# Performance work log

Hardware: AMD Instinct MI355X
Metric: run time of the kernel (lower is better)

The kernel has to match this reference:

```python
import jax, jax.numpy as jnp
import numpy as np
from jax import lax

N, C_IN, L = 32, 8, 4096
C_LAT, K_EMB, E_DIM = 64, 512, 64
KSZ, STRIDE, PAD = 4, 2, 2


def setup_inputs() -> dict:
    key = jax.random.key(0)
    ks = jax.random.split(key, 6)
    s_conv = 1.0 / np.sqrt(C_IN * KSZ)
    s_tconv = 1.0 / np.sqrt(C_LAT * KSZ)
    return {
        "x": jax.random.normal(ks[0], (N, C_IN, L), jnp.float32),
        "conv_w": jax.random.normal(ks[1], (C_LAT, C_IN, KSZ), jnp.float32) * s_conv,
        "conv_b": jax.random.normal(ks[2], (C_LAT,), jnp.float32) * s_conv,
        "codebook": jax.random.normal(ks[3], (K_EMB, E_DIM), jnp.float32),
        "tconv_w": jax.random.normal(ks[4], (C_LAT, C_IN, KSZ), jnp.float32) * s_tconv,
        "tconv_b": jax.random.normal(ks[5], (C_IN,), jnp.float32) * s_tconv,
    }


def _encode(x, conv_w, conv_b):
    z = lax.conv_general_dilated(
        x, conv_w, window_strides=(STRIDE,), padding=[(PAD, PAD)],
        dimension_numbers=("NCH", "OIH", "NCH"))
    return z + conv_b[None, :, None]


def _quantize(z_e, codebook):
    n, c, l = z_e.shape
    z_flat = z_e.transpose(0, 2, 1).reshape(-1, c)          # (n*l, c)
    z_sq = jnp.sum(z_flat * z_flat, axis=1, keepdims=True)  # (n*l, 1)
    cb_sq = jnp.sum(codebook * codebook, axis=1)            # (k,)
    dist = z_sq + cb_sq[None, :] - 2.0 * (z_flat @ codebook.T)
    indices = jnp.argmin(dist, axis=-1)                     # (n*l,)
    z_q = codebook[indices].reshape(n, l, c).transpose(0, 2, 1)
    return z_q, indices.reshape(n, l)


def _decode(z_q, tconv_w, tconv_b):
    # torch ConvTranspose1d == conv with lhs-dilated input, flipped/transposed kernel
    w_t = jnp.flip(tconv_w, -1).transpose(1, 0, 2)          # (out, in, k)
    x_rec = lax.conv_general_dilated(
        z_q, w_t, window_strides=(1,),
        padding=[(KSZ - 1 - PAD, KSZ - 1 - PAD)],
        lhs_dilation=(STRIDE,),
        dimension_numbers=("NCH", "OIH", "NCH"))
    return x_rec + tconv_b[None, :, None]


def reference(x, conv_w, conv_b, codebook, tconv_w, tconv_b):
    z_e = _encode(x, conv_w, conv_b)            # (N, C_LAT, L/2+1)
    z_q, indices = _quantize(z_e, codebook)
    x_recon = _decode(z_q, tconv_w, tconv_b)    # (N, C_IN, L)
    return x_recon, z_e, z_q, indices
```

## Files before the change

### kernel.cpp

```cpp
#include <hip/hip_runtime.h>
#include <stdint.h>

#define N_B   32
#define C_INN 8
#define L_IN  4096
#define C_LAT 64
#define K_EMB 512
#define E_DIM 64
#define L_OUT 2049
#define M_ROWS (N_B * L_OUT)

#define SZ_XREC (N_B * C_INN * L_IN)
#define SZ_ZE   (N_B * C_LAT * L_OUT)
#define OFF_XREC 0
#define OFF_ZE   (SZ_XREC)
#define OFF_ZQ   (OFF_ZE + SZ_ZE)
#define OFF_IDX  (OFF_ZQ + SZ_ZE)

typedef short short8 __attribute__((ext_vector_type(8)));
typedef float f32x4  __attribute__((ext_vector_type(4)));

__device__ __forceinline__ unsigned short rne16(float f) {
    unsigned u = __float_as_uint(f);
    return (unsigned short)((u + 0x7FFFu + ((u >> 16) & 1u)) >> 16);
}
__device__ __forceinline__ float frombits16(unsigned short h) {
    return __uint_as_float(((unsigned)h) << 16);
}
__device__ __forceinline__ unsigned orderbits(float f) {
    unsigned u = __float_as_uint(f);
    return u ^ ((unsigned)((int)u >> 31) | 0x80000000u);
}

__global__ __launch_bounds__(256) void prep_kernel(
    const float* __restrict__ cb, unsigned short* __restrict__ frag,
    float* __restrict__ cbh)
{
    const int ntile = blockIdx.x;
    const int t     = threadIdx.x;
    const int lane  = t & 63;
    const int ks    = (t >> 6) & 1;
    const int h     = t >> 7;
    const int code  = ntile * 16 + (lane & 15);
    const int k0    = ks * 32 + (lane >> 4) * 8;

    const float* src = cb + (size_t)code * E_DIM + k0;
    unsigned short out[8];
#pragma unroll
    for (int j = 0; j < 8; ++j) {
        const float v = src[j];
        const unsigned short hb = rne16(v);
        out[j] = h ? rne16(v - frombits16(hb)) : hb;
    }
    short8 v8;
#pragma unroll
    for (int j = 0; j < 8; ++j) v8[j] = (short)out[j];
    short8* dst = (short8*)(frag + (((size_t)(ntile * 2 + ks) * 2 + h) * 512 + lane * 8));
    *dst = v8;

    if (t < 16) {
        const int c2 = ntile * 16 + t;
        const float4* cp = (const float4*)(cb + (size_t)c2 * E_DIM);
        float s = 0.0f;
#pragma unroll
        for (int d = 0; d < E_DIM / 4; ++d) {
            float4 v = cp[d];
            s += v.x * v.x + v.y * v.y + v.z * v.z + v.w * v.w;
        }
        cbh[c2] = 0.5f * s;
    }
}

__global__ __launch_bounds__(256, 3) void quantize_kernel(
    const float* __restrict__ x, const float* __restrict__ conv_w,
    const float* __restrict__ conv_b, const float* __restrict__ cb,
    const unsigned short* __restrict__ frag, const float* __restrict__ cbh_ws,
    float* __restrict__ z_e, float* __restrict__ z_q,
    float* __restrict__ idx_out)
{
    __shared__ float s_z[E_DIM][66];
    __shared__ float s_cbh[K_EMB];
    __shared__ unsigned s_cand[64][69];
    __shared__ float s_znorm[64];
    __shared__ unsigned s_mstar[64];
    __shared__ unsigned long long s_final[64];
    __shared__ unsigned s_list[256];
    __shared__ int s_cnt;

    const int tid  = threadIdx.x;
    const int wave = tid >> 6;
    const int lane = tid & 63;
    const int p    = wave >> 1;
    const int h    = wave & 1;

    const bool strip_active = (blockIdx.x * 64 + p * 32) < M_ROWS;

    s_cbh[tid]       = cbh_ws[tid];
    s_cbh[tid + 256] = cbh_ws[tid + 256];
    if (tid < 64) s_final[tid] = ~0ULL;
    if (tid == 0) s_cnt = 0;

    const int  row    = lane;
    const int  r      = blockIdx.x * 64 + row;
    const bool active = (r < M_ROWS);
    const unsigned rr = active ? (unsigned)r : 0u;
    const unsigned n  = rr / 2049u;
    const unsigned tt = rr - n * 2049u;

    {
        const float* xrow = x + (size_t)n * (C_INN * L_IN);
        float xv[C_INN][4];
        const bool fast = (tt >= 1 && tt <= 2047);
        if (fast) {
#pragma unroll
            for (int ci = 0; ci < C_INN; ++ci) {
                float4 v = *(const float4*)(xrow + ci * L_IN + (2 * (int)tt - 2));
                xv[ci][0] = v.x; xv[ci][1] = v.y; xv[ci][2] = v.z; xv[ci][3] = v.w;
            }
        } else {
#pragma unroll
            for (int ci = 0; ci < C_INN; ++ci) {
#pragma unroll
                for (int k = 0; k < 4; ++k) {
                    int xi = 2 * (int)tt - 2 + k;
                    int xc = min(max(xi, 0), L_IN - 1);
                    float v = xrow[ci * L_IN + xc];
                    xv[ci][k] = (xi >= 0 && xi < L_IN) ? v : 0.0f;
                }
            }
        }
#pragma unroll
        for (int j = 0; j < 16; ++j) {
            const int c = wave * 16 + j;
            float a = conv_b[c];
#pragma unroll
            for (int ci = 0; ci < C_INN; ++ci) {
                const float* wp = conv_w + (c * C_INN + ci) * 4;
#pragma unroll
                for (int k = 0; k < 4; ++k) a += xv[ci][k] * wp[k];
            }
            s_z[c][row] = a;
        }
    }
    __syncthreads();

    if (tid < 64) {
        float s = 0.0f;
#pragma unroll 8
        for (int c = 0; c < E_DIM; ++c) {
            const float v = s_z[c][tid];
            s += v * v;
        }
        s_znorm[tid] = 0.5f * s + 1.0f;
    }

    const int m = lane & 15, q = lane >> 4;
    short8 Ah[2][2], Al[2][2];
    if (strip_active) {
#pragma unroll
        for (int st = 0; st < 2; ++st) {
            const int arow = p * 32 + st * 16 + m;
#pragma unroll
            for (int ks = 0; ks < 2; ++ks) {
#pragma unroll
                for (int j = 0; j < 8; ++j) {
                    const float v = -s_z[ks * 32 + q * 8 + j][arow];
                    const unsigned short hb = rne16(v);
                    Ah[st][ks][j] = (short)hb;
                    Al[st][ks][j] = (short)rne16(v - frombits16(hb));
                }
            }
        }
    }
    __syncthreads();

    float Kn[2][4];
#pragma unroll
    for (int st = 0; st < 2; ++st)
#pragma unroll
        for (int r4 = 0; r4 < 4; ++r4)
            Kn[st][r4] = s_znorm[p * 32 + st * 16 + q * 4 + r4];

    unsigned ca[2][4], cb2[2][4];
#pragma unroll
    for (int st = 0; st < 2; ++st)
#pragma unroll
        for (int r4 = 0; r4 < 4; ++r4) { ca[st][r4] = 0xFFFFFFFFu; cb2[st][r4] = 0xFFFFFFFFu; }

    if (strip_active) {
        const short8* B8 = (const short8*)frag;
        short8 Bc[4], Bn[4];
        {
            const int base = (h * 16) * 256 + lane;
#pragma unroll
            for (int v = 0; v < 4; ++v) Bc[v] = B8[base + v * 64];
        }

        for (int t = 0; t < 16; ++t) {
            if (t < 15) {
                const int base = (h * 16 + t + 1) * 256 + lane;
#pragma unroll
                for (int v = 0; v < 4; ++v) Bn[v] = B8[base + v * 64];
            }
            const int code = (h * 16 + t) * 16 + m;
            const float chv = s_cbh[code];

            f32x4 accA = {chv + Kn[0][0], chv + Kn[0][1], chv + Kn[0][2], chv + Kn[0][3]};
            f32x4 accB = {chv + Kn[1][0], chv + Kn[1][1], chv + Kn[1][2], chv + Kn[1][3]};
            accA = __builtin_amdgcn_mfma_f32_16x16x32_bf16(Ah[0][0], Bc[0], accA, 0, 0, 0);
            accB = __builtin_amdgcn_mfma_f32_16x16x32_bf16(Ah[1][0], Bc[0], accB, 0, 0, 0);
            accA = __builtin_amdgcn_mfma_f32_16x16x32_bf16(Ah[0][0], Bc[1], accA, 0, 0, 0);
            accB = __builtin_amdgcn_mfma_f32_16x16x32_bf16(Ah[1][0], Bc[1], accB, 0, 0, 0);
            accA = __builtin_amdgcn_mfma_f32_16x16x32_bf16(Al[0][0], Bc[0], accA, 0, 0, 0);
            accB = __builtin_amdgcn_mfma_f32_16x16x32_bf16(Al[1][0], Bc[0], accB, 0, 0, 0);
            accA = __builtin_amdgcn_mfma_f32_16x16x32_bf16(Ah[0][1], Bc[2], accA, 0, 0, 0);
            accB = __builtin_amdgcn_mfma_f32_16x16x32_bf16(Ah[1][1], Bc[2], accB, 0, 0, 0);
            accA = __builtin_amdgcn_mfma_f32_16x16x32_bf16(Ah[0][1], Bc[3], accA, 0, 0, 0);
            accB = __builtin_amdgcn_mfma_f32_16x16x32_bf16(Ah[1][1], Bc[3], accB, 0, 0, 0);
            accA = __builtin_amdgcn_mfma_f32_16x16x32_bf16(Al[0][1], Bc[2], accA, 0, 0, 0);
            accB = __builtin_amdgcn_mfma_f32_16x16x32_bf16(Al[1][1], Bc[2], accB, 0, 0, 0);

#pragma unroll
            for (int st = 0; st < 2; ++st) {
                const f32x4 acc = st ? accB : accA;
#pragma unroll
                for (int r4 = 0; r4 < 4; ++r4) {
                    const unsigned xx = (__float_as_uint(acc[r4]) & 0xFFFFFFF0u) | (unsigned)t;
                    const unsigned mx = max(ca[st][r4], xx);
                    ca[st][r4]  = min(ca[st][r4], xx);
                    cb2[st][r4] = min(cb2[st][r4], mx);
                }
            }
#pragma unroll
            for (int v = 0; v < 4; ++v) Bc[v] = Bn[v];
        }
    }

#pragma unroll
    for (int st = 0; st < 2; ++st)
#pragma unroll
        for (int r4 = 0; r4 < 4; ++r4) {
            const int rw = p * 32 + st * 16 + q * 4 + r4;
            s_cand[rw][h * 32 + 2 * m + 0] = ca[st][r4];
            s_cand[rw][h * 32 + 2 * m + 1] = cb2[st][r4];
        }
    __syncthreads();

    if (tid < 64) {
        unsigned mn = 0xFFFFFFFFu;
#pragma unroll 8
        for (int i = 0; i < 64; ++i) mn = min(mn, s_cand[tid][i]);
        s_mstar[tid] = mn & 0xFFFFFFF0u;
    }
    __syncthreads();

    {
        const int rw  = tid >> 2;
        const float thr = __uint_as_float(s_mstar[rw]) + 0.02f;
#pragma unroll
        for (int j = 0; j < 16; ++j) {
            const int sl = (tid & 3) * 16 + j;
            const unsigned cand = s_cand[rw][sl];
            const float fd = __uint_as_float(cand & 0xFFFFFFF0u);
            if (fd <= thr) {
                const unsigned code =
                    (((unsigned)(sl >> 5) * 16u + (cand & 15u)) * 16u) +
                    (unsigned)((sl >> 1) & 15);
                const int pos = atomicAdd(&s_cnt, 1);
                if (pos < 256) {
                    s_list[pos] = ((unsigned)rw << 9) | code;
                } else {
                    const float4* c4 = (const float4*)(cb + (size_t)code * E_DIM);
                    float dot = 0.0f;
#pragma unroll
                    for (int d4 = 0; d4 < 16; ++d4) {
                        const float4 cv = c4[d4];
                        dot += s_z[d4 * 4 + 0][rw] * cv.x +
                               s_z[d4 * 4 + 1][rw] * cv.y +
                               s_z[d4 * 4 + 2][rw] * cv.z +
                               s_z[d4 * 4 + 3][rw] * cv.w;
                    }
                    const float mex = s_cbh[code] - dot;
                    const unsigned long long px =
                        ((unsigned long long)orderbits(mex) << 32) | code;
                    atomicMin(&s_final[rw], px);
                }
            }
        }
    }
    __syncthreads();

    {
        const int nk = min(s_cnt, 256);
        for (int e = tid; e < nk; e += 256) {
            const unsigned ent = s_list[e];
            const int rw = (int)(ent >> 9);
            const unsigned code = ent & 511u;
            const float4* c4 = (const float4*)(cb + (size_t)code * E_DIM);
            float dot = 0.0f;
#pragma unroll
            for (int d4 = 0; d4 < 16; ++d4) {
                const float4 cv = c4[d4];
                dot += s_z[d4 * 4 + 0][rw] * cv.x +
                       s_z[d4 * 4 + 1][rw] * cv.y +
                       s_z[d4 * 4 + 2][rw] * cv.z +
                       s_z[d4 * 4 + 3][rw] * cv.w;
            }
            const float mex = s_cbh[code] - dot;
            const unsigned long long px =
                ((unsigned long long)orderbits(mex) << 32) | code;
            atomicMin(&s_final[rw], px);
        }
    }
    __syncthreads();

    if (active) {
        float* zez = z_e + (size_t)n * (C_LAT * L_OUT) + tt;
#pragma unroll
        for (int j = 0; j < 16; ++j) {
            const int c = wave * 16 + j;
            zez[(size_t)c * L_OUT] = s_z[c][row];
        }
        const unsigned fk = (unsigned)s_final[row];
        const float4* csel = (const float4*)(cb + (size_t)fk * E_DIM);
        float* zq = z_q + (size_t)n * (C_LAT * L_OUT) + tt;
#pragma unroll
        for (int j4 = 0; j4 < 4; ++j4) {
            const float4 cv = csel[wave * 4 + j4];
            const int c = wave * 16 + j4 * 4;
            zq[(size_t)(c + 0) * L_OUT] = cv.x;
            zq[(size_t)(c + 1) * L_OUT] = cv.y;
            zq[(size_t)(c + 2) * L_OUT] = cv.z;
            zq[(size_t)(c + 3) * L_OUT] = cv.w;
        }
        if (tid < 64) idx_out[r] = (float)fk;
    }
}

__global__ __launch_bounds__(128) void decode_kernel(
    const float* __restrict__ zq, const float* __restrict__ w,
    const float* __restrict__ b, float* __restrict__ xr)
{
    const int blk   = blockIdx.x;
    const int chunk = blk & 15;
    const int cog   = (blk >> 4) & 1;
    const int n     = blk >> 5;
    const int s     = chunk * 128 + threadIdx.x;
    const int co0   = cog * 4;

    const float* zn = zq + (size_t)n * (C_LAT * L_OUT) + s;
    float e[4], o[4];
#pragma unroll
    for (int j = 0; j < 4; ++j) { e[j] = b[co0 + j]; o[j] = e[j]; }

#pragma unroll 4
    for (int ci = 0; ci < C_LAT; ++ci) {
        const float z0 = zn[(size_t)ci * L_OUT];
        const float z1 = zn[(size_t)ci * L_OUT + 1];
        const float* wp = w + (ci * C_INN + co0) * 4;
#pragma unroll
        for (int j = 0; j < 4; ++j) {
            e[j] += z0 * wp[4 * j + 2] + z1 * wp[4 * j + 0];
            o[j] += z0 * wp[4 * j + 3] + z1 * wp[4 * j + 1];
        }
    }

#pragma unroll
    for (int j = 0; j < 4; ++j) {
        float* xrow = xr + ((size_t)(n * C_INN + co0 + j)) * L_IN;
        *(float2*)(xrow + 2 * s) = make_float2(e[j], o[j]);
    }
}

extern "C" void kernel_launch(void* const* d_in, const int* in_sizes, int n_in,
                              void* d_out, int out_size, void* d_ws, size_t ws_size,
                              hipStream_t stream) {
    const float* x        = (const float*)d_in[0];
    const float* conv_w   = (const float*)d_in[1];
    const float* conv_b   = (const float*)d_in[2];
    const float* codebook = (const float*)d_in[3];
    const float* tconv_w  = (const float*)d_in[4];
    const float* tconv_b  = (const float*)d_in[5];

    float* out   = (float*)d_out;
    float* x_rec = out + OFF_XREC;
    float* z_e   = out + OFF_ZE;
    float* z_q   = out + OFF_ZQ;
    float* idxs  = out + OFF_IDX;

    unsigned short* frag = (unsigned short*)d_ws;
    float*          cbh  = (float*)(frag + 65536);

    prep_kernel<<<32, 256, 0, stream>>>(codebook, frag, cbh);
    quantize_kernel<<<(M_ROWS + 63) / 64, 256, 0, stream>>>(
        x, conv_w, conv_b, codebook, frag, cbh, z_e, z_q, idxs);
    decode_kernel<<<1024, 128, 0, stream>>>(z_q, tconv_w, tconv_b, x_rec);
}
```

Baseline: 132.7 us.

## Fuse transposed-conv decode into quantize kernel with boundary fixup kernel

Moves the decoder's transposed convolution into the quantize kernel's epilogue. The selected codebook rows are staged in shared memory (reusing the candidate buffer), and each wave computes two output channels for each row pair that lies inside the block. A small fixup kernel handles the rows that straddle two blocks (the last row of each block) by re-reading z_q from global memory. This removes the separate decode pass that re-read all of z_q from HBM, at the cost of an extra sync, more work in the quantize kernel, and a second tiny launch.

```diff
diff --git a/kernel.cpp b/kernel.cpp
--- a/kernel.cpp
+++ b/kernel.cpp
@@ -75,8 +75,9 @@
     const float* __restrict__ x, const float* __restrict__ conv_w,
     const float* __restrict__ conv_b, const float* __restrict__ cb,
     const unsigned short* __restrict__ frag, const float* __restrict__ cbh_ws,
+    const float* __restrict__ tconv_w, const float* __restrict__ tconv_b,
     float* __restrict__ z_e, float* __restrict__ z_q,
-    float* __restrict__ idx_out)
+    float* __restrict__ idx_out, float* __restrict__ x_rec)
 {
     __shared__ float s_z[E_DIM][66];
     __shared__ float s_cbh[K_EMB];
@@ -100,7 +101,7 @@
     if (tid < 64) s_final[tid] = ~0ULL;
     if (tid == 0) s_cnt = 0;
 
-    const int  row    = lane;
+    const int  row    = tid & 63;
     const int  r      = blockIdx.x * 64 + row;
     const bool active = (r < M_ROWS);
     const unsigned rr = active ? (unsigned)r : 0u;
@@ -314,61 +315,92 @@
     }
     __syncthreads();
 
+    float* s_zq = (float*)&s_cand[0][0];
+    unsigned fk = 0;
+    float4 csel4[4];
+    if (active) {
+        fk = (unsigned)s_final[row];
+        const float4* csel = (const float4*)(cb + (size_t)fk * E_DIM);
+#pragma unroll
+        for (int j4 = 0; j4 < 4; ++j4) csel4[j4] = csel[wave * 4 + j4];
+#pragma unroll
+        for (int j4 = 0; j4 < 4; ++j4) {
+            const int c = wave * 16 + j4 * 4;
+            s_zq[row * 69 + c + 0] = csel4[j4].x;
+            s_zq[row * 69 + c + 1] = csel4[j4].y;
+            s_zq[row * 69 + c + 2] = csel4[j4].z;
+            s_zq[row * 69 + c + 3] = csel4[j4].w;
+        }
+    }
+    __syncthreads();
+
     if (active) {
         float* zez = z_e + (size_t)n * (C_LAT * L_OUT) + tt;
+        float* zq  = z_q + (size_t)n * (C_LAT * L_OUT) + tt;
 #pragma unroll
         for (int j = 0; j < 16; ++j) {
             const int c = wave * 16 + j;
             zez[(size_t)c * L_OUT] = s_z[c][row];
         }
-        const unsigned fk = (unsigned)s_final[row];
-        const float4* csel = (const float4*)(cb + (size_t)fk * E_DIM);
-        float* zq = z_q + (size_t)n * (C_LAT * L_OUT) + tt;
 #pragma unroll
         for (int j4 = 0; j4 < 4; ++j4) {
-            const float4 cv = csel[wave * 4 + j4];
             const int c = wave * 16 + j4 * 4;
-            zq[(size_t)(c + 0) * L_OUT] = cv.x;
-            zq[(size_t)(c + 1) * L_OUT] = cv.y;
-            zq[(size_t)(c + 2) * L_OUT] = cv.z;
-            zq[(size_t)(c + 3) * L_OUT] = cv.w;
+            zq[(size_t)(c + 0) * L_OUT] = csel4[j4].x;
+            zq[(size_t)(c + 1) * L_OUT] = csel4[j4].y;
+            zq[(size_t)(c + 2) * L_OUT] = csel4[j4].z;
+            zq[(size_t)(c + 3) * L_OUT] = csel4[j4].w;
         }
         if (tid < 64) idx_out[r] = (float)fk;
-    }
-}
-
-__global__ __launch_bounds__(128) void decode_kernel(
+
+        if (row < 63 && tt < 2048) {
+            const int co0 = wave * 2;
+            float e0 = tconv_b[co0],     o0 = e0;
+            float e1 = tconv_b[co0 + 1], o1 = e1;
+            const float* z0p = s_zq + row * 69;
+            const float* z1p = s_zq + (row + 1) * 69;
+#pragma unroll 8
+            for (int ci = 0; ci < C_LAT; ++ci) {
+                const float z0 = z0p[ci];
+                const float z1 = z1p[ci];
+                const float* wp = tconv_w + (ci * C_INN + co0) * 4;
+                e0 += z0 * wp[2] + z1 * wp[0];
+                o0 += z0 * wp[3] + z1 * wp[1];
+                e1 += z0 * wp[6] + z1 * wp[4];
+                o1 += z0 * wp[7] + z1 * wp[5];
+            }
+            float* xr0 = x_rec + ((size_t)(n * C_INN + co0)) * L_IN + 2 * tt;
+            float* xr1 = x_rec + ((size_t)(n * C_INN + co0 + 1)) * L_IN + 2 * tt;
+            *(float2*)xr0 = make_float2(e0, o0);
+            *(float2*)xr1 = make_float2(e1, o1);
+        }
+    }
+}
+
+__global__ __launch_bounds__(64) void fixup_kernel(
     const float* __restrict__ zq, const float* __restrict__ w,
     const float* __restrict__ b, float* __restrict__ xr)
 {
-    const int blk   = blockIdx.x;
-    const int chunk = blk & 15;
-    const int cog   = (blk >> 4) & 1;
-    const int n     = blk >> 5;
-    const int s     = chunk * 128 + threadIdx.x;
-    const int co0   = cog * 4;
-
-    const float* zn = zq + (size_t)n * (C_LAT * L_OUT) + s;
-    float e[4], o[4];
-#pragma unroll
-    for (int j = 0; j < 4; ++j) { e[j] = b[co0 + j]; o[j] = e[j]; }
-
-#pragma unroll 4
-    for (int ci = 0; ci < C_LAT; ++ci) {
-        const float z0 = zn[(size_t)ci * L_OUT];
-        const float z1 = zn[(size_t)ci * L_OUT + 1];
-        const float* wp = w + (ci * C_INN + co0) * 4;
-#pragma unroll
-        for (int j = 0; j < 4; ++j) {
-            e[j] += z0 * wp[4 * j + 2] + z1 * wp[4 * j + 0];
-            o[j] += z0 * wp[4 * j + 3] + z1 * wp[4 * j + 1];
-        }
-    }
-
-#pragma unroll
-    for (int j = 0; j < 4; ++j) {
-        float* xrow = xr + ((size_t)(n * C_INN + co0 + j)) * L_IN;
-        *(float2*)(xrow + 2 * s) = make_float2(e[j], o[j]);
+    const int bd = blockIdx.x;
+    const int r  = bd * 64 + 63;
+    const unsigned n  = (unsigned)r / 2049u;
+    const unsigned tt = (unsigned)r - n * 2049u;
+    if (tt >= 2048) return;
+
+    __shared__ float zz[2][64];
+    const int ci = threadIdx.x;
+    const float* zp = zq + (size_t)n * (C_LAT * L_OUT) + (size_t)ci * L_OUT + tt;
+    zz[0][ci] = zp[0];
+    zz[1][ci] = zp[1];
+    __syncthreads();
+
+    if (ci < 16) {
+        const int co = ci >> 1, par = ci & 1;
+        float a = b[co];
+        for (int c = 0; c < C_LAT; ++c) {
+            const float* wp = w + (c * C_INN + co) * 4;
+            a += zz[0][c] * wp[2 + par] + zz[1][c] * wp[0 + par];
+        }
+        xr[((size_t)(n * C_INN + co)) * L_IN + 2 * tt + par] = a;
     }
 }
 
@@ -393,6 +425,7 @@
 
     prep_kernel<<<32, 256, 0, stream>>>(codebook, frag, cbh);
     quantize_kernel<<<(M_ROWS + 63) / 64, 256, 0, stream>>>(
-        x, conv_w, conv_b, codebook, frag, cbh, z_e, z_q, idxs);
-    decode_kernel<<<1024, 128, 0, stream>>>(z_q, tconv_w, tconv_b, x_rec);
-}
+        x, conv_w, conv_b, codebook, frag, cbh, tconv_w, tconv_b,
+        z_e, z_q, idxs, x_rec);
+    fixup_kernel<<<1024, 64, 0, stream>>>(z_q, tconv_w, tconv_b, x_rec);
+}
```

After: 146.9 us. 10.7% more time.
